# Kernel tuning notes

Measured on AMD Instinct MI355X. Metric: run time of the kernel, lower is better.

## Reference

```python
import jax, jax.numpy as jnp
import numpy as np
from jax import lax

EPS = 1e-5
K = 16

def bn(x, g, b):
    # BatchNorm2d in training mode: biased batch stats over (B,H,W)
    m = x.mean(axis=(0, 2, 3), keepdims=True)
    v = x.var(axis=(0, 2, 3), keepdims=True)
    return (x - m) * lax.rsqrt(v + EPS) * g.reshape(1, -1, 1, 1) + b.reshape(1, -1, 1, 1)

def lrelu(x):
    return jnp.where(x >= 0, x, 0.01 * x)

def conv1x1(x, w, b):  # x:[B,C,N,K], w:[O,C]
    return jnp.einsum('bcnk,oc->bonk', x, w) + b.reshape(1, -1, 1, 1)

def edge_features_xyz(x, pc, k):
    B, C, N = x.shape
    xt = jnp.swapaxes(x, 1, 2)                      # [B,N,C]
    xs = jnp.sum(xt * xt, axis=2, keepdims=True)    # [B,N,1]
    dist = -2.0 * jnp.einsum('bnc,bcm->bnm', xt, x) + xs + jnp.swapaxes(xs, 1, 2)
    idx = jnp.argsort(dist, axis=2)[:, :, 1:k + 1]  # [B,N,k] skip self
    gather = jax.vmap(lambda fb, ib: fb[:, ib])     # [C,N],[N,k]->[C,N,k]
    nb = gather(x, idx)                             # [B,C,N,k]
    nb_xyz = gather(pc, idx)                        # [B,3,N,k]
    central = jnp.broadcast_to(x[..., None], (B, C, N, k))
    central_xyz = jnp.broadcast_to(pc[..., None], (B, 3, N, k))
    e_fea = jnp.concatenate([central, nb - central], axis=1)          # [B,2C,N,k]
    e_xyz = jnp.concatenate([central_xyz, nb_xyz - central_xyz], axis=1)  # [B,6,N,k]
    return e_fea, e_xyz

def forward(x, pc, fea_w, fea_b, fea_g, fea_be, xyz_w, xyz_b, xyz_g, xyz_be,
            all1_w, all1_b, all1_g, all1_be, all2_w, all2_b, all2_g, all2_be,
            inte_w, inte_b, inte_g, inte_be, c2_w, c2_b, c2_g, c2_be):
    B, Fin, N = x.shape
    k = K
    e_fea, e_xyz = edge_features_xyz(x, pc, k)      # [B,2Fin,N,k],[B,6,N,k]
    w_fea = lrelu(bn(conv1x1(e_fea, fea_w, fea_b), fea_g, fea_be))   # [B,16,N,k]
    w_xyz = lrelu(bn(conv1x1(e_xyz, xyz_w, xyz_b), xyz_g, xyz_be))   # [B,16,N,k]
    w = w_fea * w_xyz
    w = lrelu(bn(conv1x1(w, all1_w, all1_b), all1_g, all1_be))       # [B,64,N,k]
    w = lrelu(bn(conv1x1(w, all2_w, all2_b), all2_g, all2_be))       # [B,2Fin,N,k]
    w = jax.nn.softmax(w, axis=-1)
    CC = 2 * Fin
    # inte_conv_hk: Conv2d(2Fin->4Fin, kernel [1, k//2+1]) -> [B,4Fin,N,k//2]
    inte = lax.conv_general_dilated(e_fea, inte_w, (1, 1), 'VALID',
                                    dimension_numbers=('NCHW', 'OIHW', 'NCHW'))
    inte = inte + inte_b.reshape(1, -1, 1, 1)
    inte = lrelu(bn(inte, inte_g, inte_be))
    # torch reshape dance: [B,4Fin,N,k/2] -> [B,N,4Fin,k/2] -> [B,N,2Fin,2,k/2] -> [B,N,2Fin,k] -> [B,2Fin,N,k]
    inte = jnp.transpose(inte, (0, 2, 1, 3)).reshape(B, N, CC, 2, k // 2)
    inte = inte.reshape(B, N, CC, k).transpose(0, 2, 1, 3)
    inte_x = inte * w
    merge = jnp.concatenate([e_fea, inte_x], axis=3)                 # [B,2Fin,N,2k]
    # conv2: kernel [1,2k] spans full width -> contraction
    out = jnp.einsum('bcnw,ocw->bon', merge, c2_w[:, :, 0, :]) + c2_b.reshape(1, -1, 1)
    out = out[..., None]                                             # [B,2Fout,N,1]
    out = jnp.maximum(bn(out, c2_g, c2_be), 0.0)                     # ReLU
    Fout = out.shape[1] // 2
    return out.reshape(B, Fout, 2 * N)

def setup_inputs():
    B, Fin, Fout, N, k = 8, 64, 64, 2048, 16
    ks = jax.random.split(jax.random.key(0), 10)
    p = lambda i, s, sc=0.05: jax.random.normal(ks[i], s, jnp.float32) * sc
    return {
        'x': p(0, (B, Fin, N), 1.0),
        'pc': p(1, (B, 3, N), 1.0),
        'fea_w': p(2, (16, 2 * Fin)), 'fea_b': jnp.zeros(16), 'fea_g': jnp.ones(16), 'fea_be': jnp.zeros(16),
        'xyz_w': p(3, (16, 6)), 'xyz_b': jnp.zeros(16), 'xyz_g': jnp.ones(16), 'xyz_be': jnp.zeros(16),
        'all1_w': p(4, (64, 16)), 'all1_b': jnp.zeros(64), 'all1_g': jnp.ones(64), 'all1_be': jnp.zeros(64),
        'all2_w': p(5, (2 * Fin, 64)), 'all2_b': jnp.zeros(2 * Fin), 'all2_g': jnp.ones(2 * Fin), 'all2_be': jnp.zeros(2 * Fin),
        'inte_w': p(6, (4 * Fin, 2 * Fin, 1, k // 2 + 1)), 'inte_b': jnp.zeros(4 * Fin), 'inte_g': jnp.ones(4 * Fin), 'inte_be': jnp.zeros(4 * Fin),
        'c2_w': p(7, (2 * Fout, 2 * Fin, 1, 2 * k)), 'c2_b': jnp.zeros(2 * Fout), 'c2_g': jnp.ones(2 * Fout), 'c2_be': jnp.zeros(2 * Fout),
    }

def reference(x, pc, fea_w, fea_b, fea_g, fea_be, xyz_w, xyz_b, xyz_g, xyz_be,
              all1_w, all1_b, all1_g, all1_be, all2_w, all2_b, all2_g, all2_be,
              inte_w, inte_b, inte_g, inte_be, c2_w, c2_b, c2_g, c2_be):
    return forward(x, pc, fea_w, fea_b, fea_g, fea_be, xyz_w, xyz_b, xyz_g, xyz_be,
                   all1_w, all1_b, all1_g, all1_be, all2_w, all2_b, all2_g, all2_be,
                   inte_w, inte_b, inte_g, inte_be, c2_w, c2_b, c2_g, c2_be)
```

## Files before the change

kernel.cpp:

```cpp
#include <hip/hip_runtime.h>
#include <math.h>

typedef unsigned short ushort_t;

#define B_   8
#define N_   2048
#define K_   16
#define C2_  128
#define C4_  256
#define KH_  8
#define TAP_ 9
#define NK_  32768
#define EPSv 1e-5f
#define BIGF 3.0e38f
#define NMASK 2047

constexpr size_t AL(size_t x) { return (x + 255) & ~(size_t)255; }
constexpr size_t OFF_XT   = 0;
constexpr size_t OFF_IDX  = OFF_XT  + AL(4ull * B_ * N_ * 64);
constexpr size_t OFF_U1   = OFF_IDX + AL(4ull * B_ * N_ * K_);
constexpr size_t OFF_V1   = OFF_U1  + AL(4ull * B_ * 16 * N_);
constexpr size_t OFF_U2   = OFF_V1  + AL(4ull * B_ * N_ * 16);
constexpr size_t OFF_V2   = OFF_U2  + AL(4ull * B_ * 16 * N_);
constexpr size_t OFF_S    = OFF_V2  + AL(4ull * B_ * N_ * 16);
// ... 86 lines not shown
  union { float f; unsigned u; } v; v.u = h << 16; return v.f;
}
static __device__ __forceinline__ ushort_t f2bf(float f) {
  union { float f; unsigned u; } v; v.f = f;
  unsigned r = v.u + 0x7fffu + ((v.u >> 16) & 1u);
  return (ushort_t)(r >> 16);
}

__global__ __launch_bounds__(256) void zero_kernel(char* base)
{
  BASE(base);
  for (int i = threadIdx.x; i < 4096; i += 256) P_ST[i] = 0.0f;
  for (int i = threadIdx.x; i < 64; i += 256) P_PROG[i] = 0;
  __syncthreads();
  if (threadIdx.x == 0) P_PROG[0] = 1;
}

__global__ __launch_bounds__(256) void xt_kernel(char* base, const float* __restrict__ x)
{
  BASE(base);
  PROG(8);
  int b = blockIdx.x >> 5; int m0 = (blockIdx.x & 31) * 64;
  int t = threadIdx.x;
  __shared__ float tile[64 * 65];
  for (int i = t; i < 4096; i += 256) {
    int ml = i & 63, c = i >> 6;
    tile[c * 65 + ml] = x[((size_t)(b * 64 + c)) * N_ + m0 + ml];
  }
  __syncthreads();
  for (int i = t; i < 4096; i += 256) {
    int c = i & 63, ml = i >> 6;
    P_XT[((size_t)(b * N_) + m0 + ml) * 64 + c] = tile[c * 65 + ml];
  }
}

__global__ __launch_bounds__(256) void prep_kernel(char* base,
    const float* __restrict__ fea_w,
    const float* __restrict__ xyz_w, const float* __restrict__ inte_w,
    const float* __restrict__ c2_w, const float* __restrict__ all1_w,
    const float* __restrict__ all2_w)
{
  BASE(base);
  PROG(1);
  int i = blockIdx.x * 256 + threadIdx.x;
  if (i < 1024) { int o = i & 15, c = i >> 4;
    P_WU12[i] = fea_w[o * 128 + c] - fea_w[o * 128 + 64 + c]; return; }
  i -= 1024;
  if (i < 1024) { int o = i & 15, c = i >> 4;
    P_WV12[i] = fea_w[o * 128 + 64 + c]; return; }
  i -= 1024;
  if (i < 64) { int c = i & 3, o = i >> 2;
    P_WU22[i] = (c < 3) ? (xyz_w[o * 6 + c] - xyz_w[o * 6 + 3 + c]) : 0.0f; return; }
  i -= 64;
  if (i < 64) { int c = i & 3, o = i >> 2;
    P_WV22[i] = (c < 3) ? xyz_w[o * 6 + 3 + c] : 0.0f; return; }
  i -= 64;
  if (i < 16384) { int o = i & 255, c = i >> 8;
    float s = 0.0f;
    for (int t = 0; t < TAP_; t++)
      s += inte_w[(o * 128 + c) * TAP_ + t] - inte_w[(o * 128 + 64 + c) * TAP_ + t];
    P_WP2[i] = s; return; }
  i -= 16384;
  if (i < 147456) {
    int o = i & 255; int tc = i >> 8; int c = tc & 63; int tt = tc >> 6;
    P_WQ2[i] = inte_w[(o * 128 + 64 + c) * TAP_ + tt]; return; }
  i -= 147456;
  if (i < 8192) { int o = i & 127, c = i >> 7;
    float s = 0.0f;
    for (int p = 0; p < 16; p++)
      s += c2_w[(o * 128 + c) * 32 + p] - c2_w[(o * 128 + 64 + c) * 32 + p];
    P_WS2[i] = s; return; }
  i -= 8192;
  if (i < 393216) { int o = i & 127; int k = i >> 7; float v;
    if (k < 1024) { int c = k >> 4, p = k & 15; v = c2_w[(o * 128 + 64 + c) * 32 + p]; }
    else { int kr = k - 1024; int cc = kr >> 4, kk = kr & 15; v = c2_w[(o * 128 + cc) * 32 + 16 + kk]; }
    P_WC2[i] = v; return; }
  i -= 393216;
  if (i < 1024) { int c = i & 15, o = i >> 4; P_A12[i] = all1_w[o * 16 + c]; return; }
  i -= 1024;
  if (i < 8192) {
    int o = i & 127, c = i >> 7; P_A22[i] = all2_w[o * 64 + c]; return; }
}

__global__ __launch_bounds__(256) void knn_kernel(char* base,
                                                  const float* __restrict__ x)
{
  BASE(base);
  PROG(2);
  int b = blockIdx.x >> 9; int n0 = (blockIdx.x & 511) * 4;
  int t = threadIdx.x;
  __shared__ float sdist[4][N_];
  __shared__ __align__(16) float xn[4][64];
  __shared__ float sxn[4];
  {
    int nn = t >> 6, c = t & 63;
    xn[nn][c] = P_XT[((size_t)(b * N_) + n0 + nn) * 64 + c];
  }
  __syncthreads();
  if (t < 4) {
    float s = 0.0f;
    for (int c = 0; c < 64; c++) { float v = xn[t][c]; s += v * v; }
    sxn[t] = s;
  }
  __syncthreads();
  float dd[32]; float xs[8];
#pragma unroll
  for (int i = 0; i < 32; i++) dd[i] = 0.0f;
#pragma unroll
  for (int i = 0; i < 8; i++) xs[i] = 0.0f;
  const float* xbase = x + (size_t)b * 64 * N_ + (t << 3);
  for (int cq = 0; cq < 16; cq++) {
    float4 a0 = *(const float4*)&xn[0][cq * 4];
    float4 a1 = *(const float4*)&xn[1][cq * 4];
    float4 a2 = *(const float4*)&xn[2][cq * 4];
    float4 a3 = *(const float4*)&xn[3][cq * 4];
    float p[4][8];
#pragma unroll
    for (int cc = 0; cc < 4; cc++) {
      const float* xr = xbase + (size_t)(cq * 4 + cc) * N_;
      float4 u = *(const float4*)xr;
      float4 v = *(const float4*)(xr + 4);
      p[cc][0] = u.x; p[cc][1] = u.y; p[cc][2] = u.z; p[cc][3] = u.w;
      p[cc][4] = v.x; p[cc][5] = v.y; p[cc][6] = v.z; p[cc][7] = v.w;
    }
#pragma unroll
    for (int j = 0; j < 8; j++) {
      float x0 = p[0][j], x1 = p[1][j], x2 = p[2][j], x3 = p[3][j];
      xs[j] += x0 * x0 + x1 * x1 + x2 * x2 + x3 * x3;
      dd[0 * 8 + j] += a0.x * x0 + a0.y * x1 + a0.z * x2 + a0.w * x3;
      dd[1 * 8 + j] += a1.x * x0 + a1.y * x1 + a1.z * x2 + a1.w * x3;
      dd[2 * 8 + j] += a2.x * x0 + a2.y * x1 + a2.z * x2 + a2.w * x3;
      dd[3 * 8 + j] += a3.x * x0 + a3.y * x1 + a3.z * x2 + a3.w * x3;
    }
  }
  float sx0 = sxn[0], sx1 = sxn[1], sx2 = sxn[2], sx3 = sxn[3];
  int mb = t << 3;
#pragma unroll
  for (int j = 0; j < 8; j++) {
    int m = mb + j;
    float d0 = -2.0f * dd[0 * 8 + j] + sx0 + xs[j];
    float d1 = -2.0f * dd[1 * 8 + j] + sx1 + xs[j];
    float d2 = -2.0f * dd[2 * 8 + j] + sx2 + xs[j];
    float d3 = -2.0f * dd[3 * 8 + j] + sx3 + xs[j];
    sdist[0][m] = (m == n0 + 0) ? BIGF : d0;
    sdist[1][m] = (m == n0 + 1) ? BIGF : d1;
    sdist[2][m] = (m == n0 + 2) ? BIGF : d2;
    sdist[3][m] = (m == n0 + 3) ? BIGF : d3;
  }
  __syncthreads();
  int ln = t & 63; int wv = t >> 6;
  float v[32];
#pragma unroll
  for (int j = 0; j < 32; j++) v[j] = sdist[wv][ln + j * 64];
  float bv = v[0]; int bj = 0;
#pragma unroll
  for (int j = 1; j < 32; j++) { if (v[j] < bv) { bv = v[j]; bj = j; } }
  int* op = P_IDX + ((size_t)(b * N_) + n0 + wv) * K_;
  for (int it = 0; it < K_; it++) {
    float rv = bv; int ri = ln + (bj << 6);
#pragma unroll
    for (int off = 32; off > 0; off >>= 1) {
      float ov = __shfl_xor(rv, off);
      int oi = __shfl_xor(ri, off);
      if (ov < rv || (ov == rv && oi < ri)) { rv = ov; ri = oi; }
    }
    if (ln == 0) op[it] = ri;
    if ((ri & 63) == ln) {
      int slot = ri >> 6;
#pragma unroll
      for (int j = 0; j < 32; j++) v[j] = (j == slot) ? BIGF : v[j];
      bv = v[0]; bj = 0;
#pragma unroll
      for (int j = 1; j < 32; j++) { if (v[j] < bv) { bv = v[j]; bj = j; } }
    }
  }
}

__global__ __launch_bounds__(256) void point_gemm_kernel(char* base,
                                                         const float* __restrict__ pc)
{
  BASE(base);
  PROG(3);
  int b = blockIdx.x >> 6; int m0 = (blockIdx.x & 63) * 32;
  int t = threadIdx.x;
  __shared__ __align__(16) float actS[64][40];
  __shared__ float pcs[3][32];
  for (int i = t; i < 2048; i += 256) {
    int c = i & 63, mm = i >> 6;
    actS[c][mm] = P_XT[((size_t)(b * N_) + m0 + mm) * 64 + c];
  }
  if (t < 96) {
    int c = t >> 5, mm = t & 31;
    pcs[c][mm] = pc[(b * 3 + c) * N_ + m0 + mm];
  }
  __syncthreads();
  size_t bN = (size_t)(b * N_);
  {
    int og = t & 31, pg = t >> 5;
    float acc[8][4];
#pragma unroll
    for (int oi = 0; oi < 8; oi++)
#pragma unroll
      for (int pj = 0; pj < 4; pj++) acc[oi][pj] = 0.0f;
    for (int c = 0; c < 64; c++) {
      float4 a = *(const float4*)&actS[c][pg * 4];
      const float* wr = P_WP2 + c * 256 + og * 8;
      float4 w0 = *(const float4*)wr;
      float4 w1 = *(const float4*)(wr + 4);
      float av[4] = {a.x, a.y, a.z, a.w};
      float wv[8] = {w0.x, w0.y, w0.z, w0.w, w1.x, w1.y, w1.z, w1.w};
#pragma unroll
      for (int oi = 0; oi < 8; oi++)
#pragma unroll
        for (int pj = 0; pj < 4; pj++) acc[oi][pj] += wv[oi] * av[pj];
    }
#pragma unroll
    for (int pj = 0; pj < 4; pj++) {
      float* pp = P_P + (bN + m0 + pg * 4 + pj) * C4_ + og * 8;
      *(float4*)pp = make_float4(acc[0][pj], acc[1][pj], acc[2][pj], acc[3][pj]);
      *(float4*)(pp + 4) = make_float4(acc[4][pj], acc[5][pj], acc[6][pj], acc[7][pj]);
    }
  }
  {
    int og = t & 15, pg = t >> 4;
    float acc[8][2];
#pragma unroll
    for (int oi = 0; oi < 8; oi++) { acc[oi][0] = 0.0f; acc[oi][1] = 0.0f; }
    for (int c = 0; c < 64; c++) {
      float a0 = actS[c][pg * 2], a1 = actS[c][pg * 2 + 1];
      const float* wr = P_WS2 + c * 128 + og * 8;
      float4 w0 = *(const float4*)wr;
      float4 w1 = *(const float4*)(wr + 4);
      float wv[8] = {w0.x, w0.y, w0.z, w0.w, w1.x, w1.y, w1.z, w1.w};
#pragma unroll
      for (int oi = 0; oi < 8; oi++) { acc[oi][0] += wv[oi] * a0; acc[oi][1] += wv[oi] * a1; }
    }
#pragma unroll
    for (int pj = 0; pj < 2; pj++) {
      float* sp = P_Sb + (bN + m0 + pg * 2 + pj) * C2_ + og * 8;
      *(float4*)sp = make_float4(acc[0][pj], acc[1][pj], acc[2][pj], acc[3][pj]);
      *(float4*)(sp + 4) = make_float4(acc[4][pj], acc[5][pj], acc[6][pj], acc[7][pj]);
    }
  }
  {
    int o = t & 15, pg = t >> 4;
    float aU[2] = {0.0f, 0.0f}, aV[2] = {0.0f, 0.0f};
    for (int c = 0; c < 64; c++) {
      float wu = P_WU12[c * 16 + o];
      float wv = P_WV12[c * 16 + o];
      float a0 = actS[c][pg * 2], a1 = actS[c][pg * 2 + 1];
      aU[0] += wu * a0; aU[1] += wu * a1;
      aV[0] += wv * a0; aV[1] += wv * a1;
    }
    float u0 = P_WU22[o * 4], u1 = P_WU22[o * 4 + 1], u2w = P_WU22[o * 4 + 2];
    float v0 = P_WV22[o * 4], v1 = P_WV22[o * 4 + 1], v2w = P_WV22[o * 4 + 2];
#pragma unroll
    for (int pj = 0; pj < 2; pj++) {
      int m = m0 + pg * 2 + pj;
      P_U1[((b * 16 + o) << 11) + m] = aU[pj];
      P_V1[(bN + m) * 16 + o] = aV[pj];
      float p0 = pcs[0][pg * 2 + pj], p1 = pcs[1][pg * 2 + pj], p2 = pcs[2][pg * 2 + pj];
      P_U2[((b * 16 + o) << 11) + m] = u0 * p0 + u1 * p1 + u2w * p2;
      P_V2[(bN + m) * 16 + o] = v0 * p0 + v1 * p1 + v2w * p2;
    }
  }
}

__global__ __launch_bounds__(256) void stats12_kernel(char* base,
    const float* __restrict__ fea_b, const float* __restrict__ xyz_b)
{
  BASE(base);
  PROG(4);
  int b = blockIdx.x >> 7; int n0 = (blockIdx.x & 127) * 16;
  int t = threadIdx.x; int o = t & 15; int kk = t >> 4;
  float fb = fea_b[o], xb = xyz_b[o];
  float s1 = 0, q1 = 0, s2 = 0, q2 = 0;
  for (int nn = 0; nn < 16; nn++) {
    int n = n0 + nn;
    int m = P_IDX[((b << 11) + n) * K_ + kk] & NMASK;
    float a1 = fb + P_U1[((b * 16 + o) << 11) + n] + P_V1[(((size_t)(b << 11) + m) << 4) + o];
    s1 += a1; q1 += a1 * a1;
    float a2 = xb + P_U2[((b * 16 + o) << 11) + n] + P_V2[(((size_t)(b << 11) + m) << 4) + o];
    s2 += a2; q2 += a2 * a2;
  }
  __shared__ float red[256];
  red[t] = s1; __syncthreads();
  if (t < 16) { float s = 0; for (int k2 = 0; k2 < 16; k2++) s += red[k2 * 16 + t]; atomicAdd(&P_ST[ST_S1S + t], s); }
  __syncthreads();
  red[t] = q1; __syncthreads();
  if (t < 16) { float s = 0; for (int k2 = 0; k2 < 16; k2++) s += red[k2 * 16 + t]; atomicAdd(&P_ST[ST_S1Q + t], s); }
  __syncthreads();
  red[t] = s2; __syncthreads();
  if (t < 16) { float s = 0; for (int k2 = 0; k2 < 16; k2++) s += red[k2 * 16 + t]; atomicAdd(&P_ST[ST_S2S + t], s); }
  __syncthreads();
  red[t] = q2; __syncthreads();
  if (t < 16) { float s = 0; for (int k2 = 0; k2 < 16; k2++) s += red[k2 * 16 + t]; atomicAdd(&P_ST[ST_S2Q + t], s); }
}

__global__ __launch_bounds__(256) void finalize_bn_kernel(char* base,
                                   const float* __restrict__ g,
                                   const float* __restrict__ be,
                                   int sum_off, int sq_off, int sc_off, int sh_off,
                                   int nch, float inv_cnt, int kid)
{
  BASE(base);
  PROG(kid);
  int i = threadIdx.x;
  if (i < nch) {
    float mu = P_ST[sum_off + i] * inv_cnt;
    float var = fmaxf(P_ST[sq_off + i] * inv_cnt - mu * mu, 0.0f);
    float s = g[i] * rsqrtf(var + EPSv);
    P_ST[sc_off + i] = s; P_ST[sh_off + i] = be[i] - mu * s;
  }
}

__global__ __launch_bounds__(256) void w1_kernel(char* base,
    const float* __restrict__ fea_b, const float* __restrict__ xyz_b)
{
  BASE(base);
  PROG(7);
  int b = blockIdx.x >> 7; int n0 = (blockIdx.x & 127) * 16;
  int t = threadIdx.x;
  __shared__ int sidx[16 * 16];
  __shared__ __align__(16) float ol[16 * 260];
  {
    int nl = t >> 4, k = t & 15;
    sidx[nl * 16 + k] = P_IDX[((size_t)((b << 11) + n0 + nl)) * 16 + k] & NMASK;
  }
  __syncthreads();
  int c = t >> 4; int nl = t & 15; int n = n0 + nl;
  float u1 = P_U1[((b * 16 + c) << 11) + n];
  float u2 = P_U2[((b * 16 + c) << 11) + n];
  float c1 = fea_b[c] + u1, c2v = xyz_b[c] + u2;
  float s1 = P_ST[ST_B1SC + c], h1 = P_ST[ST_B1SH + c];
  float s2 = P_ST[ST_B2SC + c], h2 = P_ST[ST_B2SH + c];
  float o16[16];
#pragma unroll
  for (int kk = 0; kk < 16; kk++) {
    int m = sidx[nl * 16 + kk];
    float a1 = c1 + P_V1[(((size_t)(b << 11) + m) << 4) + c];
    a1 = lrelu(a1 * s1 + h1);
    float a2 = c2v + P_V2[(((size_t)(b << 11) + m) << 4) + c];
    a2 = lrelu(a2 * s2 + h2);
    o16[kk] = a1 * a2;
  }
  float* wp = P_W1 + ((size_t)(b * 16 + c)) * NK_ + ((size_t)n << 4);
#pragma unroll
// ... 115 lines not shown
#pragma unroll
  for (int oi = 0; oi < 8; oi++) {
    int o = og * 8 + oi;
    unsigned lo = (unsigned)f2bf(acc[oi][0]) | ((unsigned)f2bf(acc[oi][1]) << 16);
    unsigned hi = (unsigned)f2bf(acc[oi][2]) | ((unsigned)f2bf(acc[oi][3]) << 16);
    *(uint2*)(dst + o * 16) = make_uint2(lo, hi);
    float r0 = bf2f(lo & 0xffffu), r1 = bf2f(lo >> 16);
    float r2 = bf2f(hi & 0xffffu), r3 = bf2f(hi >> 16);
    psum[oi] = r0 + r1 + r2 + r3;
    qsum[oi] = r0 * r0 + r1 * r1 + r2 * r2 + r3 * r3;
  }
  __syncthreads();
  float* redS = hS;
#pragma unroll
  for (int oi = 0; oi < 8; oi++) redS[(og * 8 + oi) * 16 + cg] = psum[oi];
  __syncthreads();
  if (t < 128) {
    float s = 0.0f;
    for (int j = 0; j < 16; j++) s += redS[t * 16 + j];
    atomicAdd(&P_ST[ST_S4S + t], s);
  }
  __syncthreads();
#pragma unroll
  for (int oi = 0; oi < 8; oi++) redS[(og * 8 + oi) * 16 + cg] = qsum[oi];
  __syncthreads();
  if (t < 128) {
    float s = 0.0f;
    for (int j = 0; j < 16; j++) s += redS[t * 16 + j];
    atomicAdd(&P_ST[ST_S4Q + t], s);
  }
}

__global__ __launch_bounds__(256) void softfuse_kernel(char* base)
{
  BASE(base);
  PROG(13);
  int rid = blockIdx.x * 256 + threadIdx.x;
  int cc = rid & 127; int r = rid >> 7;
  float s = P_ST[ST_B4SC + cc], h = P_ST[ST_B4SH + cc];
  size_t base_off = (size_t)r * 2048 + cc * 16;
  const ushort_t* pa = P_A4 + base_off;
  uint4 u0 = *(const uint4*)pa;
  uint4 u1 = *(const uint4*)(pa + 8);
  unsigned ws[8] = {u0.x, u0.y, u0.z, u0.w, u1.x, u1.y, u1.z, u1.w};
  float v[16];
#pragma unroll
  for (int j = 0; j < 8; j++) {
    union { float f; unsigned u; } lo, hi;
    lo.u = ws[j] << 16; hi.u = ws[j] & 0xffff0000u;
    v[2 * j] = lo.f; v[2 * j + 1] = hi.f;
  }
  float mx = -BIGF;
#pragma unroll
  for (int i = 0; i < 16; i++) {
    float y = lrelu(v[i] * s + h);
    v[i] = y; mx = fmaxf(mx, y);
  }
  float sum = 0.0f;
#pragma unroll
  for (int i = 0; i < 16; i++) { float e = expf(v[i] - mx); v[i] = e; sum += e; }
  float inv = (sum > 0.0f) ? 1.0f / sum : 0.0f;
#pragma unroll
  for (int i = 0; i < 16; i++) v[i] = bf2f((unsigned)f2bf(v[i] * inv));
  float s5a = P_ST[ST_B5SC + cc * 2],     h5a = P_ST[ST_B5SH + cc * 2];
  float s5b = P_ST[ST_B5SC + cc * 2 + 1], h5b = P_ST[ST_B5SH + cc * 2 + 1];
  const ushort_t* itp = P_IT + base_off;
  uint4 i0 = *(const uint4*)itp;
  uint4 i1 = *(const uint4*)(itp + 8);
  unsigned iw[8] = {i0.x, i0.y, i0.z, i0.w, i1.x, i1.y, i1.z, i1.w};
  unsigned mw[8];
#pragma unroll
  for (int j = 0; j < 8; j++) {
    union { float f; unsigned u; } il, ih;
    il.u = iw[j] << 16; ih.u = iw[j] & 0xffff0000u;
    float s5 = (j < 4) ? s5a : s5b;
    float h5 = (j < 4) ? h5a : h5b;
    float m0 = lrelu(il.f * s5 + h5) * v[2 * j];
    float m1 = lrelu(ih.f * s5 + h5) * v[2 * j + 1];
    mw[j] = (unsigned)f2bf(m0) | ((unsigned)f2bf(m1) << 16);
  }
  ushort_t* mp = P_M + base_off;
  *(uint4*)mp = make_uint4(mw[0], mw[1], mw[2], mw[3]);
  *(uint4*)(mp + 8) = make_uint4(mw[4], mw[5], mw[6], mw[7]);
}

__global__ __launch_bounds__(256) void qgemm_kernel(char* base)
{
  BASE(base);
  PROG(14);
  int b = blockIdx.x >> 6; int m0 = (blockIdx.x & 63) * 32;
  int t = threadIdx.x;
  int og = t & 31;
  int pg = t >> 5;
  __shared__ __align__(16) float actS[64][40];
  for (int i = t; i < 2048; i += 256) {
    int c = i & 63, mm = i >> 6;
    actS[c][mm] = P_XT[((size_t)(b * N_) + m0 + mm) * 64 + c];
  }
  __syncthreads();
  int m = m0 + pg * 4;
  for (int t9 = 0; t9 < TAP_; t9++) {
    const float* wbase = P_WQ2 + ((size_t)t9 * 64) * 256 + og * 8;
    float acc[8][4];
#pragma unroll
    for (int oi = 0; oi < 8; oi++)
#pragma unroll
      for (int pj = 0; pj < 4; pj++) acc[oi][pj] = 0.0f;
    for (int kc = 0; kc < 64; kc++) {
      float4 a = *(const float4*)&actS[kc][pg * 4];
      const float* wr = wbase + (size_t)kc * 256;
      float4 w0 = *(const float4*)wr;
      float4 w1 = *(const float4*)(wr + 4);
      float av[4] = {a.x, a.y, a.z, a.w};
      float wv[8] = {w0.x, w0.y, w0.z, w0.w, w1.x, w1.y, w1.z, w1.w};
#pragma unroll
      for (int oi = 0; oi < 8; oi++)
#pragma unroll
        for (int pj = 0; pj < 4; pj++)
          acc[oi][pj] += wv[oi] * av[pj];
    }
#pragma unroll
    for (int pj = 0; pj < 4; pj++) {
      ushort_t* qp = P_QB + ((size_t)(b * N_ + m + pj) * TAP_ + t9) * C4_ + og * 8;
      unsigned u0 = (unsigned)f2bf(acc[0][pj]) | ((unsigned)f2bf(acc[1][pj]) << 16);
      unsigned u1 = (unsigned)f2bf(acc[2][pj]) | ((unsigned)f2bf(acc[3][pj]) << 16);
      unsigned u2 = (unsigned)f2bf(acc[4][pj]) | ((unsigned)f2bf(acc[5][pj]) << 16);
      unsigned u3 = (unsigned)f2bf(acc[6][pj]) | ((unsigned)f2bf(acc[7][pj]) << 16);
      *(uint4*)qp = make_uint4(u0, u1, u2, u3);
    }
  }
}

__global__ __launch_bounds__(256) void inte_fused_kernel(char* base,
                                                         const float* __restrict__ inte_b)
{
  BASE(base);
  PROG(15);
  int b = blockIdx.x >> 9; int n0 = (blockIdx.x & 511) * 4;
  int t = threadIdx.x; int o = t;
  __shared__ int sidx[4][16];
  if (t < 64) sidx[t >> 4][t & 15] = P_IDX[((size_t)(b * N_) + n0 + (t >> 4)) * K_ + (t & 15)] & NMASK;
  __syncthreads();
  float bias = inte_b[o];
  float ssum = 0.0f, ssq = 0.0f;
  for (int nn = 0; nn < 4; nn++) {
    int n = n0 + nn;
    float bse = bias + P_P[((size_t)(b * N_) + n) * C4_ + o];
    float acc[8];
#pragma unroll
    for (int j = 0; j < 8; j++) acc[j] = bse;
    for (int p = 0; p < 16; p++) {
      const ushort_t* qr = P_QB + (size_t)(b * N_ + sidx[nn][p]) * TAP_ * C4_ + o;
#pragma unroll
      for (int tt = 0; tt < TAP_; tt++) {
        int j = p - tt;
        if (j >= 0 && j < 8) acc[j] += bf2f(((unsigned)qr[tt * C4_]) << 16 >> 16 << 16 >> 16);
      }
    }
    ushort_t* ip = P_IT + ((size_t)(b * N_) + n) * 2048 + o * 8;
#pragma unroll
    for (int j = 0; j < 8; j++) { float v = acc[j]; ip[j] = f2bf(v); ssum += v; ssq += v * v; }
  }
  atomicAdd(&P_ST[ST_S5S + o], ssum);
  atomicAdd(&P_ST[ST_S5Q + o], ssq);
}

__global__ __launch_bounds__(256) void final_conv_kernel(char* base)
{
  BASE(base);
  PROG(17);
  int ks = blockIdx.x & 1;
  int tile = (blockIdx.x >> 1) & 31; int b = blockIdx.x >> 6;
  int n0 = tile * 64;
  int t = threadIdx.x;
  int cg4 = (t & 15) * 4;
  int obase = (t >> 4) * 8;
  __shared__ __align__(16) float tileS[128 * 68];
  __shared__ int sidxT[16 * 64];
  for (int i = t; i < 1024; i += 256) {
    int cl = i & 63, p = i >> 6;
    sidxT[p * 64 + cl] = P_IDX[((size_t)(b * N_) + n0 + cl) * K_ + p] & NMASK;
  }
  float acc[32];
#pragma unroll
  for (int i = 0; i < 32; i++) acc[i] = 0.0f;
  int kbeg = ks * 1536;
  for (int k0 = kbeg; k0 < kbeg + 1536; k0 += 128) {
    __syncthreads();
    if (k0 < 1024) {
      int c0 = k0 >> 4;
      int cl = t & 63; int pg = t >> 6;
      for (int pp = 0; pp < 4; pp++) {
        int p = pg * 4 + pp;
        int m = sidxT[p * 64 + cl];
        const float* xp = P_XT + ((size_t)(b * N_) + m) * 64 + c0;
        float4 v0 = *(const float4*)xp;
        float4 v1 = *(const float4*)(xp + 4);
        tileS[(0 * 16 + p) * 68 + cl] = v0.x;
        tileS[(1 * 16 + p) * 68 + cl] = v0.y;
        tileS[(2 * 16 + p) * 68 + cl] = v0.z;
        tileS[(3 * 16 + p) * 68 + cl] = v0.w;
        tileS[(4 * 16 + p) * 68 + cl] = v1.x;
        tileS[(5 * 16 + p) * 68 + cl] = v1.y;
        tileS[(6 * 16 + p) * 68 + cl] = v1.z;
        tileS[(7 * 16 + p) * 68 + cl] = v1.w;
      }
    } else {
      int cl = t & 63; int kg = t >> 6;
      size_t rb = ((size_t)(b * N_) + n0 + cl) * 2048 + (size_t)(k0 - 1024) + kg * 32;
      const ushort_t* mp = P_M + rb;
      for (int j8 = 0; j8 < 4; j8++) {
        uint4 u = *(const uint4*)(mp + j8 * 8);
        unsigned ws[4] = {u.x, u.y, u.z, u.w};
#pragma unroll
        for (int q = 0; q < 4; q++) {
          union { float f; unsigned uu; } lo, hi;
          lo.uu = ws[q] << 16; hi.uu = ws[q] & 0xffff0000u;
          int kc = kg * 32 + j8 * 8 + q * 2;
          tileS[kc * 68 + cl] = lo.f;
          tileS[(kc + 1) * 68 + cl] = hi.f;
        }
      }
    }
    __syncthreads();
    for (int kc = 0; kc < 128; kc++) {
      float4 a = *(const float4*)&tileS[kc * 68 + cg4];
      const float* wr = P_WC2 + (size_t)(k0 + kc) * C2_ + obase;
      float4 w0 = *(const float4*)wr;
      float4 w1 = *(const float4*)(wr + 4);
      float av[4] = {a.x, a.y, a.z, a.w};
      float wv[8] = {w0.x, w0.y, w0.z, w0.w, w1.x, w1.y, w1.z, w1.w};
#pragma unroll
      for (int oi = 0; oi < 8; oi++)
#pragma unroll
        for (int cj = 0; cj < 4; cj++)
          acc[oi * 4 + cj] += wv[oi] * av[cj];
    }
  }
#pragma unroll
  for (int cj = 0; cj < 4; cj++) {
    float* op = P_PART + ((size_t)ks * B_ * N_ + (size_t)b * N_ + n0 + cg4 + cj) * C2_ + obase;
    *(float4*)op = make_float4(acc[0 * 4 + cj], acc[1 * 4 + cj], acc[2 * 4 + cj], acc[3 * 4 + cj]);
    *(float4*)(op + 4) = make_float4(acc[4 * 4 + cj], acc[5 * 4 + cj], acc[6 * 4 + cj], acc[7 * 4 + cj]);
  }
}

__global__ __launch_bounds__(256) void reduce_stats_kernel(char* base,
                                                           const float* __restrict__ c2_b)
{
  BASE(base);
  PROG(18);
  int r0 = blockIdx.x * 32;
  int t = threadIdx.x; int o = t & 127; int h = t >> 7;
  const size_t STRIDE = (size_t)B_ * N_ * C2_;
  float cb = c2_b[o];
  float s = 0, q = 0;
  for (int r = r0 + h; r < r0 + 32; r += 2) {
    size_t off = (size_t)r * C2_ + o;
    float v = cb + P_Sb[off] + P_PART[off] + P_PART[STRIDE + off];
    P_OUT2[off] = v;
    s += v; q += v * v;
  }
  __shared__ float rs[256], rq[256];
  rs[t] = s; rq[t] = q; __syncthreads();
  if (t < 128) {
    atomicAdd(&P_ST[ST_S6S + o], rs[t] + rs[t + 128]);
    atomicAdd(&P_ST[ST_S6Q + o], rq[t] + rq[t + 128]);
  }
}

__global__ __launch_bounds__(256) void output_kernel(char* base, float* __restrict__ out)
{
  BASE(base);
  PROG(20);
  int b = blockIdx.x >> 6; int n0 = (blockIdx.x & 63) * 32;
  int t = threadIdx.x;
  __shared__ float tile[32 * 133];
  for (int i = t; i < 4096; i += 256) {
    int o = i & 127, nl = i >> 7;
    float v = P_OUT2[((size_t)(b * N_) + n0 + nl) * C2_ + o];
    v = v * P_ST[ST_B6SC + o] + P_ST[ST_B6SH + o];
    tile[nl * 133 + o] = fmaxf(v, 0.0f);
  }
  __syncthreads();
  for (int i = t; i < 4096; i += 256) {
    int nl = i & 31, o = i >> 5;
    out[(((size_t)b * 64 + (o >> 1)) * 2 + (o & 1)) * 2048 + n0 + nl] = tile[nl * 133 + o];
  }
}

__global__ void diag_kernel(char* base, float* __restrict__ out)
{
  BASE(base);
  const int expctd[22] = {1, 2253, 4096, 512, 1024, 1, 1, 1024, 256, 1, 4096,
                          0, 1, 8192, 512, 4096, 1, 512, 512, 1, 512, 0};
  int t = threadIdx.x;
  int bad = 99;
  if (t < 22 && P_PROG[t] != expctd[t]) bad = t;
#pragma unroll
  for (int off = 32; off > 0; off >>= 1) {
    int ob = __shfl_xor(bad, off);
    if (ob < bad) bad = ob;
  }
  if (t == 0 && bad != 99) out[0] = 100.0f + 10.0f * (float)bad;
}

__global__ void code_kernel(float* __restrict__ out, float code)
{
  if (threadIdx.x == 0 && blockIdx.x == 0) out[0] = code;
}

extern "C" void kernel_launch(void* const* d_in, const int* in_sizes, int n_in,
                              void* d_out, int out_size, void* d_ws, size_t ws_size,
                              hipStream_t stream) {
  const float* x      = (const float*)d_in[0];
  const float* pc     = (const float*)d_in[1];
  const float* fea_w  = (const float*)d_in[2];
  const float* fea_b  = (const float*)d_in[3];
  const float* fea_g  = (const float*)d_in[4];
  const float* fea_be = (const float*)d_in[5];
  const float* xyz_w  = (const float*)d_in[6];
  const float* xyz_b  = (const float*)d_in[7];
  const float* xyz_g  = (const float*)d_in[8];
  const float* xyz_be = (const float*)d_in[9];
  const float* all1_w = (const float*)d_in[10];
  const float* all1_b = (const float*)d_in[11];
  const float* all1_g = (const float*)d_in[12];
  const float* all1_be= (const float*)d_in[13];
  const float* all2_w = (const float*)d_in[14];
  const float* all2_b = (const float*)d_in[15];
  const float* all2_g = (const float*)d_in[16];
  const float* all2_be= (const float*)d_in[17];
  const float* inte_w = (const float*)d_in[18];
  const float* inte_b = (const float*)d_in[19];
  const float* inte_g = (const float*)d_in[20];
  const float* inte_be= (const float*)d_in[21];
  const float* c2_w   = (const float*)d_in[22];
  const float* c2_b   = (const float*)d_in[23];
  const float* c2_g   = (const float*)d_in[24];
  const float* c2_be  = (const float*)d_in[25];
  float* out = (float*)d_out;
  (void)in_sizes; (void)n_in; (void)out_size; (void)d_ws; (void)ws_size;

  if (g_pool_mem == nullptr) {
    code_kernel<<<1, 64, 0, stream>>>(out, 500.0f);
    return;
  }
  char* base = g_pool_mem;

  zero_kernel<<<1, 256, 0, stream>>>(base);
  xt_kernel<<<256, 256, 0, stream>>>(base, x);
  prep_kernel<<<2253, 256, 0, stream>>>(base, fea_w, xyz_w, inte_w, c2_w, all1_w, all2_w);
  knn_kernel<<<4096, 256, 0, stream>>>(base, x);
  point_gemm_kernel<<<512, 256, 0, stream>>>(base, pc);
  stats12_kernel<<<1024, 256, 0, stream>>>(base, fea_b, xyz_b);
  finalize_bn_kernel<<<1, 256, 0, stream>>>(base, fea_g, fea_be, ST_S1S, ST_S1Q, ST_B1SC, ST_B1SH, 16, 1.0f / 262144.0f, 5);
  finalize_bn_kernel<<<1, 256, 0, stream>>>(base, xyz_g, xyz_be, ST_S2S, ST_S2Q, ST_B2SC, ST_B2SH, 16, 1.0f / 262144.0f, 6);
  w1_kernel<<<1024, 256, 0, stream>>>(base, fea_b, xyz_b);
  finalize_bn3_kernel<<<1, 256, 0, stream>>>(base, all1_b, all1_g, all1_be);
  a4_kernel<<<4096, 256, 0, stream>>>(base, all1_b, all2_b);
  finalize_bn_kernel<<<1, 256, 0, stream>>>(base, all2_g, all2_be, ST_S4S, ST_S4Q, ST_B4SC, ST_B4SH, 128, 1.0f / 262144.0f, 12);
  qgemm_kernel<<<512, 256, 0, stream>>>(base);
  inte_fused_kernel<<<4096, 256, 0, stream>>>(base, inte_b);
  finalize_bn_kernel<<<1, 256, 0, stream>>>(base, inte_g, inte_be, ST_S5S, ST_S5Q, ST_B5SC, ST_B5SH, 256, 1.0f / 131072.0f, 16);
  softfuse_kernel<<<8192, 256, 0, stream>>>(base);
  final_conv_kernel<<<512, 256, 0, stream>>>(base);
  reduce_stats_kernel<<<512, 256, 0, stream>>>(base, c2_b);
  finalize_bn_kernel<<<1, 256, 0, stream>>>(base, c2_g, c2_be, ST_S6S, ST_S6Q, ST_B6SC, ST_B6SH, 128, 1.0f / 16384.0f, 19);
  output_kernel<<<512, 256, 0, stream>>>(base, out);
  diag_kernel<<<1, 64, 0, stream>>>(base, out);
}
```

Before: 1.229 ms.

## Merge kNN, point GEMM and Q GEMM into one heterogeneous launch

Combines the kNN kernel, the per-point GEMM kernel and the Q-tap GEMM kernel into a single phaseA kernel. Block IDs are interleaved so that every fifth block runs a GEMM task and the rest run kNN tasks. This lets the lighter GEMM work overlap with the long kNN blocks and removes two launch boundaries. Shared memory is now a union sized for the largest role, which may reduce occupancy for the GEMM blocks, and the diagnostic counters are updated to match.

```diff
diff --git a/kernel.cpp b/kernel.cpp
--- a/kernel.cpp
+++ b/kernel.cpp
@@ -192,187 +192,234 @@
     int o = i & 127, c = i >> 7; P_A22[i] = all2_w[o * 64 + c]; return; }
 }
 
-__global__ __launch_bounds__(256) void knn_kernel(char* base,
-                                                  const float* __restrict__ x)
+__global__ __launch_bounds__(256) void phaseA_kernel(char* base,
+                                                     const float* __restrict__ x,
+                                                     const float* __restrict__ pc)
 {
   BASE(base);
   PROG(2);
-  int b = blockIdx.x >> 9; int n0 = (blockIdx.x & 511) * 4;
+  __shared__ __align__(16) char smem[33824];
+  int bid = blockIdx.x;
   int t = threadIdx.x;
-  __shared__ float sdist[4][N_];
-  __shared__ __align__(16) float xn[4][64];
-  __shared__ float sxn[4];
+  if (bid % 5 != 0) {
+    int kb = bid - bid / 5 - 1;
+    int b = kb >> 9; int n0 = (kb & 511) * 4;
+    float (*sdist)[N_] = (float(*)[N_])smem;
+    float (*xn)[64]    = (float(*)[64])(smem + 32768);
+    float* sxn         = (float*)(smem + 32768 + 1024);
+    {
+      int nn = t >> 6, c = t & 63;
+      xn[nn][c] = P_XT[((size_t)(b * N_) + n0 + nn) * 64 + c];
+    }
+    __syncthreads();
+    if (t < 4) {
+      float s = 0.0f;
+      for (int c = 0; c < 64; c++) { float v = xn[t][c]; s += v * v; }
+      sxn[t] = s;
+    }
+    __syncthreads();
+    float dd[32]; float xs[8];
+#pragma unroll
+    for (int i = 0; i < 32; i++) dd[i] = 0.0f;
+#pragma unroll
+    for (int i = 0; i < 8; i++) xs[i] = 0.0f;
+    const float* xbase = x + (size_t)b * 64 * N_ + (t << 3);
+    for (int cq = 0; cq < 16; cq++) {
+      float4 a0 = *(const float4*)&xn[0][cq * 4];
+      float4 a1 = *(const float4*)&xn[1][cq * 4];
+      float4 a2 = *(const float4*)&xn[2][cq * 4];
+      float4 a3 = *(const float4*)&xn[3][cq * 4];
+      float p[4][8];
+#pragma unroll
+      for (int cc = 0; cc < 4; cc++) {
+        const float* xr = xbase + (size_t)(cq * 4 + cc) * N_;
+        float4 u = *(const float4*)xr;
+        float4 v = *(const float4*)(xr + 4);
+        p[cc][0] = u.x; p[cc][1] = u.y; p[cc][2] = u.z; p[cc][3] = u.w;
+        p[cc][4] = v.x; p[cc][5] = v.y; p[cc][6] = v.z; p[cc][7] = v.w;
+      }
+#pragma unroll
+      for (int j = 0; j < 8; j++) {
+        float x0 = p[0][j], x1 = p[1][j], x2 = p[2][j], x3 = p[3][j];
+        xs[j] += x0 * x0 + x1 * x1 + x2 * x2 + x3 * x3;
+        dd[0 * 8 + j] += a0.x * x0 + a0.y * x1 + a0.z * x2 + a0.w * x3;
+        dd[1 * 8 + j] += a1.x * x0 + a1.y * x1 + a1.z * x2 + a1.w * x3;
+        dd[2 * 8 + j] += a2.x * x0 + a2.y * x1 + a2.z * x2 + a2.w * x3;
+        dd[3 * 8 + j] += a3.x * x0 + a3.y * x1 + a3.z * x2 + a3.w * x3;
+      }
+    }
+    float sx0 = sxn[0], sx1 = sxn[1], sx2 = sxn[2], sx3 = sxn[3];
+    int mb = t << 3;
+#pragma unroll
+    for (int j = 0; j < 8; j++) {
+      int m = mb + j;
+      float d0 = -2.0f * dd[0 * 8 + j] + sx0 + xs[j];
+      float d1 = -2.0f * dd[1 * 8 + j] + sx1 + xs[j];
+      float d2 = -2.0f * dd[2 * 8 + j] + sx2 + xs[j];
+      float d3 = -2.0f * dd[3 * 8 + j] + sx3 + xs[j];
+      sdist[0][m] = (m == n0 + 0) ? BIGF : d0;
+      sdist[1][m] = (m == n0 + 1) ? BIGF : d1;
+      sdist[2][m] = (m == n0 + 2) ? BIGF : d2;
+      sdist[3][m] = (m == n0 + 3) ? BIGF : d3;
+    }
+    __syncthreads();
+    int ln = t & 63; int wv = t >> 6;
+    float v[32];
+#pragma unroll
+    for (int j = 0; j < 32; j++) v[j] = sdist[wv][ln + j * 64];
+    float bv = v[0]; int bj = 0;
+#pragma unroll
+    for (int j = 1; j < 32; j++) { if (v[j] < bv) { bv = v[j]; bj = j; } }
+    int* op = P_IDX + ((size_t)(b * N_) + n0 + wv) * K_;
+    for (int it = 0; it < K_; it++) {
+      float rv = bv; int ri = ln + (bj << 6);
+#pragma unroll
+      for (int off = 32; off > 0; off >>= 1) {
+        float ov = __shfl_xor(rv, off);
+        int oi = __shfl_xor(ri, off);
+        if (ov < rv || (ov == rv && oi < ri)) { rv = ov; ri = oi; }
+      }
+      if (ln == 0) op[it] = ri;
+      if ((ri & 63) == ln) {
+        int slot = ri >> 6;
+#pragma unroll
+        for (int j = 0; j < 32; j++) v[j] = (j == slot) ? BIGF : v[j];
+        bv = v[0]; bj = 0;
+#pragma unroll
+        for (int j = 1; j < 32; j++) { if (v[j] < bv) { bv = v[j]; bj = j; } }
+      }
+    }
+    return;
+  }
+  int s = bid / 5;
+  if (s < 512) {
+    int b = s >> 6; int m0 = (s & 63) * 32;
+    float (*actS)[40] = (float(*)[40])smem;
+    float (*pcs)[32]  = (float(*)[32])(smem + 10240);
+    for (int i = t; i < 2048; i += 256) {
+      int c = i & 63, mm = i >> 6;
+      actS[c][mm] = P_XT[((size_t)(b * N_) + m0 + mm) * 64 + c];
+    }
+    if (t < 96) {
+      int c = t >> 5, mm = t & 31;
+      pcs[c][mm] = pc[(b * 3 + c) * N_ + m0 + mm];
+    }
+    __syncthreads();
+    size_t bN = (size_t)(b * N_);
+    {
+      int og = t & 31, pg = t >> 5;
+      float acc[8][4];
+#pragma unroll
+      for (int oi = 0; oi < 8; oi++)
+#pragma unroll
+        for (int pj = 0; pj < 4; pj++) acc[oi][pj] = 0.0f;
+      for (int c = 0; c < 64; c++) {
+        float4 a = *(const float4*)&actS[c][pg * 4];
+        const float* wr = P_WP2 + c * 256 + og * 8;
+        float4 w0 = *(const float4*)wr;
+        float4 w1 = *(const float4*)(wr + 4);
+        float av[4] = {a.x, a.y, a.z, a.w};
+        float wv[8] = {w0.x, w0.y, w0.z, w0.w, w1.x, w1.y, w1.z, w1.w};
+#pragma unroll
+        for (int oi = 0; oi < 8; oi++)
+#pragma unroll
+          for (int pj = 0; pj < 4; pj++) acc[oi][pj] += wv[oi] * av[pj];
+      }
+#pragma unroll
+      for (int pj = 0; pj < 4; pj++) {
+        float* pp = P_P + (bN + m0 + pg * 4 + pj) * C4_ + og * 8;
+        *(float4*)pp = make_float4(acc[0][pj], acc[1][pj], acc[2][pj], acc[3][pj]);
+        *(float4*)(pp + 4) = make_float4(acc[4][pj], acc[5][pj], acc[6][pj], acc[7][pj]);
+      }
+    }
+    {
+      int og = t & 15, pg = t >> 4;
+      float acc[8][2];
+#pragma unroll
+      for (int oi = 0; oi < 8; oi++) { acc[oi][0] = 0.0f; acc[oi][1] = 0.0f; }
+      for (int c = 0; c < 64; c++) {
+        float a0 = actS[c][pg * 2], a1 = actS[c][pg * 2 + 1];
+        const float* wr = P_WS2 + c * 128 + og * 8;
+        float4 w0 = *(const float4*)wr;
+        float4 w1 = *(const float4*)(wr + 4);
+        float wv[8] = {w0.x, w0.y, w0.z, w0.w, w1.x, w1.y, w1.z, w1.w};
+#pragma unroll
+        for (int oi = 0; oi < 8; oi++) { acc[oi][0] += wv[oi] * a0; acc[oi][1] += wv[oi] * a1; }
+      }
+#pragma unroll
+      for (int pj = 0; pj < 2; pj++) {
+        float* sp = P_Sb + (bN + m0 + pg * 2 + pj) * C2_ + og * 8;
+        *(float4*)sp = make_float4(acc[0][pj], acc[1][pj], acc[2][pj], acc[3][pj]);
+        *(float4*)(sp + 4) = make_float4(acc[4][pj], acc[5][pj], acc[6][pj], acc[7][pj]);
+      }
+    }
+    {
+      int o = t & 15, pg = t >> 4;
+      float aU[2] = {0.0f, 0.0f}, aV[2] = {0.0f, 0.0f};
+      for (int c = 0; c < 64; c++) {
+        float wu = P_WU12[c * 16 + o];
+        float wv = P_WV12[c * 16 + o];
+        float a0 = actS[c][pg * 2], a1 = actS[c][pg * 2 + 1];
+        aU[0] += wu * a0; aU[1] += wu * a1;
+        aV[0] += wv * a0; aV[1] += wv * a1;
+      }
+      float u0 = P_WU22[o * 4], u1 = P_WU22[o * 4 + 1], u2w = P_WU22[o * 4 + 2];
+      float v0 = P_WV22[o * 4], v1 = P_WV22[o * 4 + 1], v2w = P_WV22[o * 4 + 2];
+#pragma unroll
+      for (int pj = 0; pj < 2; pj++) {
+        int m = m0 + pg * 2 + pj;
+        P_U1[((b * 16 + o) << 11) + m] = aU[pj];
+        P_V1[(bN + m) * 16 + o] = aV[pj];
+        float p0 = pcs[0][pg * 2 + pj], p1 = pcs[1][pg * 2 + pj], p2 = pcs[2][pg * 2 + pj];
+        P_U2[((b * 16 + o) << 11) + m] = u0 * p0 + u1 * p1 + u2w * p2;
+        P_V2[(bN + m) * 16 + o] = v0 * p0 + v1 * p1 + v2w * p2;
+      }
+    }
+    return;
+  }
   {
-    int nn = t >> 6, c = t & 63;
-    xn[nn][c] = P_XT[((size_t)(b * N_) + n0 + nn) * 64 + c];
-  }
-  __syncthreads();
-  if (t < 4) {
-    float s = 0.0f;
-    for (int c = 0; c < 64; c++) { float v = xn[t][c]; s += v * v; }
-    sxn[t] = s;
-  }
-  __syncthreads();
-  float dd[32]; float xs[8];
-#pragma unroll
-  for (int i = 0; i < 32; i++) dd[i] = 0.0f;
-#pragma unroll
-  for (int i = 0; i < 8; i++) xs[i] = 0.0f;
-  const float* xbase = x + (size_t)b * 64 * N_ + (t << 3);
-  for (int cq = 0; cq < 16; cq++) {
-    float4 a0 = *(const float4*)&xn[0][cq * 4];
-    float4 a1 = *(const float4*)&xn[1][cq * 4];
-    float4 a2 = *(const float4*)&xn[2][cq * 4];
-    float4 a3 = *(const float4*)&xn[3][cq * 4];
-    float p[4][8];
-#pragma unroll
-    for (int cc = 0; cc < 4; cc++) {
-      const float* xr = xbase + (size_t)(cq * 4 + cc) * N_;
-      float4 u = *(const float4*)xr;
-      float4 v = *(const float4*)(xr + 4);
-      p[cc][0] = u.x; p[cc][1] = u.y; p[cc][2] = u.z; p[cc][3] = u.w;
-      p[cc][4] = v.x; p[cc][5] = v.y; p[cc][6] = v.z; p[cc][7] = v.w;
-    }
-#pragma unroll
-    for (int j = 0; j < 8; j++) {
-      float x0 = p[0][j], x1 = p[1][j], x2 = p[2][j], x3 = p[3][j];
-      xs[j] += x0 * x0 + x1 * x1 + x2 * x2 + x3 * x3;
-      dd[0 * 8 + j] += a0.x * x0 + a0.y * x1 + a0.z * x2 + a0.w * x3;
-      dd[1 * 8 + j] += a1.x * x0 + a1.y * x1 + a1.z * x2 + a1.w * x3;
-      dd[2 * 8 + j] += a2.x * x0 + a2.y * x1 + a2.z * x2 + a2.w * x3;
-      dd[3 * 8 + j] += a3.x * x0 + a3.y * x1 + a3.z * x2 + a3.w * x3;
-    }
-  }
-  float sx0 = sxn[0], sx1 = sxn[1], sx2 = sxn[2], sx3 = sxn[3];
-  int mb = t << 3;
-#pragma unroll
-  for (int j = 0; j < 8; j++) {
-    int m = mb + j;
-    float d0 = -2.0f * dd[0 * 8 + j] + sx0 + xs[j];
-    float d1 = -2.0f * dd[1 * 8 + j] + sx1 + xs[j];
-    float d2 = -2.0f * dd[2 * 8 + j] + sx2 + xs[j];
-    float d3 = -2.0f * dd[3 * 8 + j] + sx3 + xs[j];
-    sdist[0][m] = (m == n0 + 0) ? BIGF : d0;
-    sdist[1][m] = (m == n0 + 1) ? BIGF : d1;
-    sdist[2][m] = (m == n0 + 2) ? BIGF : d2;
-    sdist[3][m] = (m == n0 + 3) ? BIGF : d3;
-  }
-  __syncthreads();
-  int ln = t & 63; int wv = t >> 6;
-  float v[32];
-#pragma unroll
-  for (int j = 0; j < 32; j++) v[j] = sdist[wv][ln + j * 64];
-  float bv = v[0]; int bj = 0;
-#pragma unroll
-  for (int j = 1; j < 32; j++) { if (v[j] < bv) { bv = v[j]; bj = j; } }
-  int* op = P_IDX + ((size_t)(b * N_) + n0 + wv) * K_;
-  for (int it = 0; it < K_; it++) {
-    float rv = bv; int ri = ln + (bj << 6);
-#pragma unroll
-    for (int off = 32; off > 0; off >>= 1) {
-      float ov = __shfl_xor(rv, off);
-      int oi = __shfl_xor(ri, off);
-      if (ov < rv || (ov == rv && oi < ri)) { rv = ov; ri = oi; }
-    }
-    if (ln == 0) op[it] = ri;
-    if ((ri & 63) == ln) {
-      int slot = ri >> 6;
-#pragma unroll
-      for (int j = 0; j < 32; j++) v[j] = (j == slot) ? BIGF : v[j];
-      bv = v[0]; bj = 0;
-#pragma unroll
-      for (int j = 1; j < 32; j++) { if (v[j] < bv) { bv = v[j]; bj = j; } }
-    }
-  }
-}
-
-__global__ __launch_bounds__(256) void point_gemm_kernel(char* base,
-                                                         const float* __restrict__ pc)
-{
-  BASE(base);
-  PROG(3);
-  int b = blockIdx.x >> 6; int m0 = (blockIdx.x & 63) * 32;
-  int t = threadIdx.x;
-  __shared__ __align__(16) float actS[64][40];
-  __shared__ float pcs[3][32];
-  for (int i = t; i < 2048; i += 256) {
-    int c = i & 63, mm = i >> 6;
-    actS[c][mm] = P_XT[((size_t)(b * N_) + m0 + mm) * 64 + c];
-  }
-  if (t < 96) {
-    int c = t >> 5, mm = t & 31;
-    pcs[c][mm] = pc[(b * 3 + c) * N_ + m0 + mm];
-  }
-  __syncthreads();
-  size_t bN = (size_t)(b * N_);
-  {
-    int og = t & 31, pg = t >> 5;
-    float acc[8][4];
-#pragma unroll
-    for (int oi = 0; oi < 8; oi++)
-#pragma unroll
-      for (int pj = 0; pj < 4; pj++) acc[oi][pj] = 0.0f;
-    for (int c = 0; c < 64; c++) {
-      float4 a = *(const float4*)&actS[c][pg * 4];
-      const float* wr = P_WP2 + c * 256 + og * 8;
-      float4 w0 = *(const float4*)wr;
-      float4 w1 = *(const float4*)(wr + 4);
-      float av[4] = {a.x, a.y, a.z, a.w};
-      float wv[8] = {w0.x, w0.y, w0.z, w0.w, w1.x, w1.y, w1.z, w1.w};
+    int q = s - 512;
+    int b = q >> 6; int m0 = (q & 63) * 32;
+    float (*actS)[40] = (float(*)[40])smem;
+    for (int i = t; i < 2048; i += 256) {
+      int c = i & 63, mm = i >> 6;
+      actS[c][mm] = P_XT[((size_t)(b * N_) + m0 + mm) * 64 + c];
+    }
+    __syncthreads();
+    int og = t & 31;
+    int pg = t >> 5;
+    int m = m0 + pg * 4;
+    for (int t9 = 0; t9 < TAP_; t9++) {
+      const float* wbase = P_WQ2 + ((size_t)t9 * 64) * 256 + og * 8;
+      float acc[8][4];
 #pragma unroll
       for (int oi = 0; oi < 8; oi++)
 #pragma unroll
-        for (int pj = 0; pj < 4; pj++) acc[oi][pj] += wv[oi] * av[pj];
-    }
-#pragma unroll
-    for (int pj = 0; pj < 4; pj++) {
-      float* pp = P_P + (bN + m0 + pg * 4 + pj) * C4_ + og * 8;
-      *(float4*)pp = make_float4(acc[0][pj], acc[1][pj], acc[2][pj], acc[3][pj]);
-      *(float4*)(pp + 4) = make_float4(acc[4][pj], acc[5][pj], acc[6][pj], acc[7][pj]);
-    }
-  }
-  {
-    int og = t & 15, pg = t >> 4;
-    float acc[8][2];
-#pragma unroll
-    for (int oi = 0; oi < 8; oi++) { acc[oi][0] = 0.0f; acc[oi][1] = 0.0f; }
-    for (int c = 0; c < 64; c++) {
-      float a0 = actS[c][pg * 2], a1 = actS[c][pg * 2 + 1];
-      const float* wr = P_WS2 + c * 128 + og * 8;
-      float4 w0 = *(const float4*)wr;
-      float4 w1 = *(const float4*)(wr + 4);
-      float wv[8] = {w0.x, w0.y, w0.z, w0.w, w1.x, w1.y, w1.z, w1.w};
-#pragma unroll
-      for (int oi = 0; oi < 8; oi++) { acc[oi][0] += wv[oi] * a0; acc[oi][1] += wv[oi] * a1; }
-    }
-#pragma unroll
-    for (int pj = 0; pj < 2; pj++) {
-      float* sp = P_Sb + (bN + m0 + pg * 2 + pj) * C2_ + og * 8;
-      *(float4*)sp = make_float4(acc[0][pj], acc[1][pj], acc[2][pj], acc[3][pj]);
-      *(float4*)(sp + 4) = make_float4(acc[4][pj], acc[5][pj], acc[6][pj], acc[7][pj]);
-    }
-  }
-  {
-    int o = t & 15, pg = t >> 4;
-    float aU[2] = {0.0f, 0.0f}, aV[2] = {0.0f, 0.0f};
-    for (int c = 0; c < 64; c++) {
-      float wu = P_WU12[c * 16 + o];
-      float wv = P_WV12[c * 16 + o];
-      float a0 = actS[c][pg * 2], a1 = actS[c][pg * 2 + 1];
-      aU[0] += wu * a0; aU[1] += wu * a1;
-      aV[0] += wv * a0; aV[1] += wv * a1;
-    }
-    float u0 = P_WU22[o * 4], u1 = P_WU22[o * 4 + 1], u2w = P_WU22[o * 4 + 2];
-    float v0 = P_WV22[o * 4], v1 = P_WV22[o * 4 + 1], v2w = P_WV22[o * 4 + 2];
-#pragma unroll
-    for (int pj = 0; pj < 2; pj++) {
-      int m = m0 + pg * 2 + pj;
-      P_U1[((b * 16 + o) << 11) + m] = aU[pj];
-      P_V1[(bN + m) * 16 + o] = aV[pj];
-      float p0 = pcs[0][pg * 2 + pj], p1 = pcs[1][pg * 2 + pj], p2 = pcs[2][pg * 2 + pj];
-      P_U2[((b * 16 + o) << 11) + m] = u0 * p0 + u1 * p1 + u2w * p2;
-      P_V2[(bN + m) * 16 + o] = v0 * p0 + v1 * p1 + v2w * p2;
-    }
+        for (int pj = 0; pj < 4; pj++) acc[oi][pj] = 0.0f;
+      for (int kc = 0; kc < 64; kc++) {
+        float4 a = *(const float4*)&actS[kc][pg * 4];
+        const float* wr = wbase + (size_t)kc * 256;
+        float4 w0 = *(const float4*)wr;
+        float4 w1 = *(const float4*)(wr + 4);
+        float av[4] = {a.x, a.y, a.z, a.w};
+        float wv[8] = {w0.x, w0.y, w0.z, w0.w, w1.x, w1.y, w1.z, w1.w};
+#pragma unroll
+        for (int oi = 0; oi < 8; oi++)
+#pragma unroll
+          for (int pj = 0; pj < 4; pj++)
+            acc[oi][pj] += wv[oi] * av[pj];
+      }
+#pragma unroll
+      for (int pj = 0; pj < 4; pj++) {
+        ushort_t* qp = P_QB + ((size_t)(b * N_ + m + pj) * TAP_ + t9) * C4_ + og * 8;
+        unsigned u0 = (unsigned)f2bf(acc[0][pj]) | ((unsigned)f2bf(acc[1][pj]) << 16);
+        unsigned u1 = (unsigned)f2bf(acc[2][pj]) | ((unsigned)f2bf(acc[3][pj]) << 16);
+        unsigned u2 = (unsigned)f2bf(acc[4][pj]) | ((unsigned)f2bf(acc[5][pj]) << 16);
+        unsigned u3 = (unsigned)f2bf(acc[6][pj]) | ((unsigned)f2bf(acc[7][pj]) << 16);
+        *(uint4*)qp = make_uint4(u0, u1, u2, u3);
+      }
+    }
+    return;
   }
 }
 
@@ -654,53 +701,6 @@
   ushort_t* mp = P_M + base_off;
   *(uint4*)mp = make_uint4(mw[0], mw[1], mw[2], mw[3]);
   *(uint4*)(mp + 8) = make_uint4(mw[4], mw[5], mw[6], mw[7]);
-}
-
-__global__ __launch_bounds__(256) void qgemm_kernel(char* base)
-{
-  BASE(base);
-  PROG(14);
-  int b = blockIdx.x >> 6; int m0 = (blockIdx.x & 63) * 32;
-  int t = threadIdx.x;
-  int og = t & 31;
-  int pg = t >> 5;
-  __shared__ __align__(16) float actS[64][40];
-  for (int i = t; i < 2048; i += 256) {
-    int c = i & 63, mm = i >> 6;
-    actS[c][mm] = P_XT[((size_t)(b * N_) + m0 + mm) * 64 + c];
-  }
-  __syncthreads();
-  int m = m0 + pg * 4;
-  for (int t9 = 0; t9 < TAP_; t9++) {
-    const float* wbase = P_WQ2 + ((size_t)t9 * 64) * 256 + og * 8;
-    float acc[8][4];
-#pragma unroll
-    for (int oi = 0; oi < 8; oi++)
-#pragma unroll
-      for (int pj = 0; pj < 4; pj++) acc[oi][pj] = 0.0f;
-    for (int kc = 0; kc < 64; kc++) {
-      float4 a = *(const float4*)&actS[kc][pg * 4];
-      const float* wr = wbase + (size_t)kc * 256;
-      float4 w0 = *(const float4*)wr;
-      float4 w1 = *(const float4*)(wr + 4);
-      float av[4] = {a.x, a.y, a.z, a.w};
-      float wv[8] = {w0.x, w0.y, w0.z, w0.w, w1.x, w1.y, w1.z, w1.w};
-#pragma unroll
-      for (int oi = 0; oi < 8; oi++)
-#pragma unroll
-        for (int pj = 0; pj < 4; pj++)
-          acc[oi][pj] += wv[oi] * av[pj];
-    }
-#pragma unroll
-    for (int pj = 0; pj < 4; pj++) {
-      ushort_t* qp = P_QB + ((size_t)(b * N_ + m + pj) * TAP_ + t9) * C4_ + og * 8;
-      unsigned u0 = (unsigned)f2bf(acc[0][pj]) | ((unsigned)f2bf(acc[1][pj]) << 16);
-      unsigned u1 = (unsigned)f2bf(acc[2][pj]) | ((unsigned)f2bf(acc[3][pj]) << 16);
-      unsigned u2 = (unsigned)f2bf(acc[4][pj]) | ((unsigned)f2bf(acc[5][pj]) << 16);
-      unsigned u3 = (unsigned)f2bf(acc[6][pj]) | ((unsigned)f2bf(acc[7][pj]) << 16);
-      *(uint4*)qp = make_uint4(u0, u1, u2, u3);
-    }
-  }
 }
 
 __global__ __launch_bounds__(256) void inte_fused_kernel(char* base,
@@ -864,8 +864,8 @@
 __global__ void diag_kernel(char* base, float* __restrict__ out)
 {
   BASE(base);
-  const int expctd[22] = {1, 2253, 4096, 512, 1024, 1, 1, 1024, 256, 1, 4096,
-                          0, 1, 8192, 512, 4096, 1, 512, 512, 1, 512, 0};
+  const int expctd[22] = {1, 2253, 5120, 0, 1024, 1, 1, 1024, 256, 1, 4096,
+                          0, 1, 8192, 0, 4096, 1, 512, 512, 1, 512, 0};
   int t = threadIdx.x;
   int bad = 99;
   if (t < 22 && P_PROG[t] != expctd[t]) bad = t;
@@ -923,8 +923,7 @@
   zero_kernel<<<1, 256, 0, stream>>>(base);
   xt_kernel<<<256, 256, 0, stream>>>(base, x);
   prep_kernel<<<2253, 256, 0, stream>>>(base, fea_w, xyz_w, inte_w, c2_w, all1_w, all2_w);
-  knn_kernel<<<4096, 256, 0, stream>>>(base, x);
-  point_gemm_kernel<<<512, 256, 0, stream>>>(base, pc);
+  phaseA_kernel<<<5120, 256, 0, stream>>>(base, x, pc);
   stats12_kernel<<<1024, 256, 0, stream>>>(base, fea_b, xyz_b);
   finalize_bn_kernel<<<1, 256, 0, stream>>>(base, fea_g, fea_be, ST_S1S, ST_S1Q, ST_B1SC, ST_B1SH, 16, 1.0f / 262144.0f, 5);
   finalize_bn_kernel<<<1, 256, 0, stream>>>(base, xyz_g, xyz_be, ST_S2S, ST_S2Q, ST_B2SC, ST_B2SH, 16, 1.0f / 262144.0f, 6);
@@ -932,7 +931,6 @@
   finalize_bn3_kernel<<<1, 256, 0, stream>>>(base, all1_b, all1_g, all1_be);
   a4_kernel<<<4096, 256, 0, stream>>>(base, all1_b, all2_b);
   finalize_bn_kernel<<<1, 256, 0, stream>>>(base, all2_g, all2_be, ST_S4S, ST_S4Q, ST_B4SC, ST_B4SH, 128, 1.0f / 262144.0f, 12);
-  qgemm_kernel<<<512, 256, 0, stream>>>(base);
   inte_fused_kernel<<<4096, 256, 0, stream>>>(base, inte_b);
   finalize_bn_kernel<<<1, 256, 0, stream>>>(base, inte_g, inte_be, ST_S5S, ST_S5Q, ST_B5SC, ST_B5SH, 256, 1.0f / 131072.0f, 16);
   softfuse_kernel<<<8192, 256, 0, stream>>>(base);
```

After: 1.193 ms. -2.9%, faster.
